# Performance work log

Measured on AMD Instinct MI355X. Metric: run time of the kernel, lower is better.

Reference implementation:

```python
import jax, jax.numpy as jnp
import numpy as np

N_NODES, N_EDGES, NNZ = 50000, 5000, 250000
IN_DIM, EDGE_DIM, N_HEADS, D_HEAD = 256, 256, 8, 64
OC = N_HEADS * D_HEAD  # out_channel = 512
EPS = 1e-5


def _segment_softmax(scores, seg, num_segments):
    # scores: [nnz, h]; softmax over entries sharing the same segment id
    m = jax.ops.segment_max(scores, seg, num_segments=num_segments)
    ex = jnp.exp(scores - m[seg])
    s = jax.ops.segment_sum(ex, seg, num_segments=num_segments)
    return ex / s[seg]


def _batchnorm(x, g, b):
    # BatchNorm1d in training mode: batch stats, biased variance
    mu = x.mean(axis=0)
    var = x.var(axis=0)
    return (x - mu) * jax.lax.rsqrt(var + EPS) * g + b


def setup_inputs() -> dict:
    key = jax.random.key(0)
    ks = jax.random.split(key, 26)
    W = lambda i, shape: (jax.random.normal(ks[i], shape, jnp.float32) * 0.05)
    inp = {
        "q": jax.random.normal(ks[0], (N_NODES, IN_DIM), jnp.float32),
        "k": jax.random.normal(ks[1], (N_NODES, IN_DIM), jnp.float32),
        "v": jax.random.normal(ks[2], (N_NODES, IN_DIM), jnp.float32),
        "edge_feat": jax.random.normal(ks[3], (N_EDGES, EDGE_DIM), jnp.float32),
        "Wq_n2h": W(4, (IN_DIM, OC)),
        "Wk_n2h": W(5, (IN_DIM, OC)),
        "Wv_n2h": W(6, (IN_DIM, OC)),
        "Wo_n2h": W(7, (OC, OC)),
        "We": W(8, (EDGE_DIM, IN_DIM)),
        "Wq_h2n": W(9, (IN_DIM, OC)),
        "Wk_h2n": W(10, (OC, OC)),
        "Wv_h2n": W(11, (OC, OC)),
        "Wo_h2n": W(12, (OC, OC)),
        "W1": W(13, (OC, 4 * OC)),
        "b1": jnp.zeros((4 * OC,), jnp.float32),
        "W2": W(14, (4 * OC, OC)),
        "b2": jnp.zeros((OC,), jnp.float32),
        "Wres": W(15, (IN_DIM, OC)),
        "g1": jnp.ones((OC,), jnp.float32),
        "beta1": jnp.zeros((OC,), jnp.float32),
        "g2": jnp.ones((OC,), jnp.float32),
        "beta2": jnp.zeros((OC,), jnp.float32),
        "node_ids": jax.random.randint(ks[16], (NNZ,), 0, N_NODES, jnp.int32),
        "hyperedge_ids": jax.random.randint(ks[17], (NNZ,), 0, N_EDGES, jnp.int32),
    }
    return inp


def reference(q, k, v, edge_feat, Wq_n2h, Wk_n2h, Wv_n2h, Wo_n2h, We,
              Wq_h2n, Wk_h2n, Wv_h2n, Wo_h2n, W1, b1, W2, b2, Wres,
              g1, beta1, g2, beta2, node_ids, hyperedge_ids):
    N, E = q.shape[0], edge_feat.shape[0]
    h, d = N_HEADS, D_HEAD
    scale = 1.0 / np.sqrt(d).astype(np.float32)

    # ---- node -> hyperedge attention (Q,V from node feats k; K from edge feats) ----
    edge_in = edge_feat @ We                                   # [E, in_dim]
    Q1 = (k @ Wq_n2h).reshape(N, h, d)
    K1 = (edge_in @ Wk_n2h).reshape(E, h, d)
    V1 = (k @ Wv_n2h).reshape(N, h, d)
    s1 = (Q1[node_ids] * K1[hyperedge_ids]).sum(-1) * scale    # [nnz, h]
    w1 = _segment_softmax(s1, hyperedge_ids, E)
    he = jax.ops.segment_sum(V1[node_ids] * w1[..., None], hyperedge_ids,
                             num_segments=E)                    # [E, h, d]
    he = he.reshape(E, h * d) @ Wo_n2h                          # [E, OC]

    # ---- hyperedge -> node attention (Q from node feats q; K,V from updated edges) ----
    Q2 = (q @ Wq_h2n).reshape(N, h, d)
    K2 = (he @ Wk_h2n).reshape(E, h, d)
    V2 = (he @ Wv_h2n).reshape(E, h, d)
    s2 = (Q2[node_ids] * K2[hyperedge_ids]).sum(-1) * scale
    w2 = _segment_softmax(s2, node_ids, N)
    nu = jax.ops.segment_sum(V2[hyperedge_ids] * w2[..., None], node_ids,
                             num_segments=N)                    # [N, h, d]
    nu = nu.reshape(N, h * d) @ Wo_h2n                          # [N, OC]

    # ---- residual + BN + FFN + residual + BN ----
    x = nu + q @ Wres
    x = _batchnorm(x, g1, beta1)
    ffn = jax.nn.gelu(x @ W1 + b1, approximate=False) @ W2 + b2
    return _batchnorm(x + ffn, g2, beta2)
```

## Files before the change

kernel.cpp:

```cpp
#include <hip/hip_runtime.h>
#include <math.h>
#include <stdint.h>

#define N_NODESC 50000
#define N_EDGESC 5000
#define NNZC     250000
#define IN_DIMC  256
#define OCC      512
#define NHC      8
#define EPSBN    1e-5f

typedef __attribute__((ext_vector_type(8))) short short8;
typedef __attribute__((ext_vector_type(4))) float f32x4;
typedef __attribute__((ext_vector_type(4))) unsigned short u16x4;
typedef unsigned short u16;

__device__ __forceinline__ u16 f2b(float f) {
    union { float f; unsigned u; } v; v.f = f;
    unsigned r = v.u + 0x7fffu + ((v.u >> 16) & 1u);
    return (u16)(r >> 16);
}

__device__ __forceinline__ void gload16(const u16* g, u16* l) {
    __builtin_amdgcn_global_load_lds(
        (const __attribute__((address_space(1))) unsigned int*)g,
        (__attribute__((address_space(3))) unsigned int*)l, 16, 0, 0);
}

__global__ __launch_bounds__(256)
void gemm_mfma(const u16* __restrict__ A, const u16* __restrict__ Bt,
               int M, int N, int K,
               const float* __restrict__ bias, int act,
               const float* resF, float* outF, u16* outB)
{
    __shared__ u16 As[128 * 64];
    __shared__ u16 Bs[128 * 64];
    const int tid  = threadIdx.x;
    const int wid  = tid >> 6, lane = tid & 63;
    const int wr   = wid >> 1, wc = wid & 1;
    const int m0   = blockIdx.y * 128, n0 = blockIdx.x * 128;

    f32x4 acc[4][4] = {};

    const int srow   = wid * 32 + (lane >> 3);
    const int schunk = (lane & 7) ^ ((lane >> 3) & 7);
    const int nk = K >> 6;

    for (int kt = 0; kt < nk; ++kt) {
        const int kb = kt * 64;
#pragma unroll
        for (int j = 0; j < 4; j++) {
            int gr = m0 + srow + j * 8;
            if (gr >= M) gr = M - 1;
            gload16(A + (size_t)gr * K + kb + schunk * 8, &As[(wid * 32 + j * 8) * 64]);
        }
#pragma unroll
        for (int j = 0; j < 4; j++) {
            int r = srow + j * 8;
            gload16(Bt + (size_t)(n0 + r) * K + kb + schunk * 8, &Bs[(wid * 32 + j * 8) * 64]);
        }
        __syncthreads();
#pragma unroll
        for (int ks = 0; ks < 2; ++ks) {
            short8 af[4], bfr[4];
#pragma unroll
            for (int mi = 0; mi < 4; mi++) {
                int r  = wr * 64 + mi * 16 + (lane & 15);
                int pc = ((lane >> 4) + ks * 4) ^ (r & 7);
                af[mi] = *(const short8*)&As[r * 64 + pc * 8];
            }
#pragma unroll
            for (int ni = 0; ni < 4; ni++) {
                int r  = wc * 64 + ni * 16 + (lane & 15);
                int pc = ((lane >> 4) + ks * 4) ^ (r & 7);
                bfr[ni] = *(const short8*)&Bs[r * 64 + pc * 8];
            }
#pragma unroll
            for (int mi = 0; mi < 4; mi++)
#pragma unroll
                for (int ni = 0; ni < 4; ni++)
                    acc[mi][ni] = __builtin_amdgcn_mfma_f32_16x16x32_bf16(
                        af[mi], bfr[ni], acc[mi][ni], 0, 0, 0);
        }
        __syncthreads();
    }

#pragma unroll
    for (int mi = 0; mi < 4; mi++) {
#pragma unroll
        for (int j = 0; j < 4; j++) {
            int row = m0 + wr * 64 + mi * 16 + (lane >> 4) * 4 + j;
            if (row >= M) continue;
#pragma unroll
            for (int ni = 0; ni < 4; ni++) {
                int col = n0 + wc * 64 + ni * 16 + (lane & 15);
                float v = acc[mi][ni][j];
                if (bias) v += bias[col];
                if (act)  v = 0.5f * v * (1.f + erff(v * 0.70710678118654752f));
                size_t o = (size_t)row * N + col;
                if (resF) v += resF[o];
                if (outF) outF[o] = v;
                if (outB) outB[o] = f2b(v);
            }
        }
    }
}

__global__ __launch_bounds__(256)
void wcast_kernel(const float* __restrict__ W, u16* __restrict__ Wt, int K, int N)
{
    __shared__ float t[32][33];
    int k0 = blockIdx.y * 32, n0 = blockIdx.x * 32;
    int tx = threadIdx.x & 31, ty = threadIdx.x >> 5;
    for (int i = ty; i < 32; i += 8)
        t[i][tx] = W[(size_t)(k0 + i) * N + n0 + tx];
    __syncthreads();
    for (int i = ty; i < 32; i += 8)
        Wt[(size_t)(n0 + i) * K + k0 + tx] = f2b(t[tx][i]);
}

__global__ __launch_bounds__(256)
void cast_kernel(const float* __restrict__ in, u16* __restrict__ out, int n)
{
    int i = (blockIdx.x * 256 + threadIdx.x) * 4;
    if (i >= n) return;
    const float4 v = *(const float4*)(in + i);
    u16x4 o; o.x = f2b(v.x); o.y = f2b(v.y); o.z = f2b(v.z); o.w = f2b(v.w);
    *(u16x4*)(out + i) = o;
}

__device__ __forceinline__ unsigned f32_order(float f) {
    unsigned u = __float_as_uint(f);
    return (u & 0x80000000u) ? ~u : (u | 0x80000000u);
}
__device__ __forceinline__ float f32_unorder(unsigned u) {
    unsigned b = (u & 0x80000000u) ? (u & 0x7FFFFFFFu) : ~u;
    return __uint_as_float(b);
}

__global__ __launch_bounds__(64)
void score_kernel(const float* __restrict__ Qm, const int* __restrict__ qids,
                  const float* __restrict__ Km, const int* __restrict__ kids,
                  const int* __restrict__ segids,
                  float* __restrict__ sout, unsigned* __restrict__ segM)
{
    int i = blockIdx.x;
    int lane = threadIdx.x;
    const float* qp = Qm + (size_t)qids[i] * OCC;
    const float* kp = Km + (size_t)kids[i] * OCC;
    float prod[NHC];
#pragma unroll
    for (int j = 0; j < NHC; j++)
        prod[j] = qp[j * 64 + lane] * kp[j * 64 + lane];
#pragma unroll
    for (int j = 0; j < NHC; j++) {
        float v = prod[j];
        for (int o = 32; o > 0; o >>= 1) v += __shfl_xor(v, o, 64);
        prod[j] = v;
    }
    if (lane < NHC) {
        float s = 0.f;
#pragma unroll
        for (int j = 0; j < NHC; j++) if (lane == j) s = prod[j];
        s *= 0.125f;
        sout[(size_t)i * NHC + lane] = s;
        atomicMax(segM + (size_t)segids[i] * NHC + lane, f32_order(s));
    }
}

__global__ __launch_bounds__(256)
void expsum_kernel(float* __restrict__ s, const int* __restrict__ segids,
                   const unsigned* __restrict__ segM, float* __restrict__ segS,
                   int n)
{
    int idx = blockIdx.x * blockDim.x + threadIdx.x;
    if (idx >= n) return;
    int i = idx >> 3, j = idx & 7;
    int seg = segids[i];
    float m = f32_unorder(segM[(size_t)seg * NHC + j]);
    float e = expf(s[idx] - m);
    s[idx] = e;
    atomicAdd(segS + (size_t)seg * NHC + j, e);
}

__global__ __launch_bounds__(64)
void scatter_kernel(const float* __restrict__ Vm, const int* __restrict__ vids,
                    const int* __restrict__ dids, const float* __restrict__ ex,
                    float* acc)
{
    int i = blockIdx.x;
    int lane = threadIdx.x;
    const float* vp = Vm + (size_t)vids[i] * OCC;
    float* ap = acc + (size_t)dids[i] * OCC;
    const float* exr = ex + (size_t)i * NHC;
#pragma unroll
    for (int j = 0; j < NHC; j++)
        atomicAdd(ap + j * 64 + lane, vp[j * 64 + lane] * exr[j]);
}

__global__ __launch_bounds__(256)
void norm_seg_b_kernel(const float* __restrict__ acc, const float* __restrict__ segS,
                       u16* __restrict__ outb, int n)
{
    int idx = blockIdx.x * blockDim.x + threadIdx.x;
    if (idx >= n) return;
    int r = idx >> 9;
    int c = idx & 511;
    float s = segS[(size_t)r * NHC + (c >> 6)];
    outb[idx] = f2b((s > 0.f) ? acc[idx] / s : 0.f);
}

__global__ __launch_bounds__(256)
void bn_stats_kernel(const float* __restrict__ x, float* sums, float* sumsq,
                     int rows)
{
    int t = threadIdx.x;
    float s0 = 0.f, s1 = 0.f, q0 = 0.f, q1 = 0.f;
    for (int r = blockIdx.x; r < rows; r += gridDim.x) {
        const float* xp = x + (size_t)r * OCC;
        float a = xp[t], b = xp[t + 256];
        s0 += a; q0 += a * a;
        s1 += b; q1 += b * b;
    }
    atomicAdd(&sums[t], s0);
    atomicAdd(&sums[t + 256], s1);
    atomicAdd(&sumsq[t], q0);
    atomicAdd(&sumsq[t + 256], q1);
}

__global__ __launch_bounds__(256)
void bn_apply_kernel(const float* __restrict__ x, const float* __restrict__ sums,
                     const float* __restrict__ sumsq, const float* __restrict__ g,
                     const float* __restrict__ b, float* y, int rows)
{
    int idx = blockIdx.x * blockDim.x + threadIdx.x;
    if (idx >= rows * OCC) return;
    int c = idx & 511;
    float inv_n = 1.f / (float)rows;
    float mu = sums[c] * inv_n;
    float var = sumsq[c] * inv_n - mu * mu;
    float rstd = rsqrtf(var + EPSBN);
    y[idx] = (x[idx] - mu) * rstd * g[c] + b[c];
}


static inline void launch_mfma(const u16* A, const u16* Bt, int M, int N, int K,
                               const float* bias, int act, const float* resF,
                               float* outF, u16* outB, hipStream_t s)
{
    dim3 g(N / 128, (M + 127) / 128);
    hipLaunchKernelGGL(gemm_mfma, g, dim3(256), 0, s, A, Bt, M, N, K,
                       bias, act, resF, outF, outB);
}
static inline void launch_wcast(const float* W, u16* Wt, int K, int N, hipStream_t s)
{
    hipLaunchKernelGGL(wcast_kernel, dim3(N / 32, K / 32), dim3(256), 0, s, W, Wt, K, N);
}
static inline void launch_cast(const float* in, u16* out, int n, hipStream_t s)
{
    hipLaunchKernelGGL(cast_kernel, dim3((n / 4 + 255) / 256), dim3(256), 0, s, in, out, n);
}

extern "C" void kernel_launch(void* const* d_in, const int* in_sizes, int n_in,
                              void* d_out, int out_size, void* d_ws, size_t ws_size,
                              hipStream_t stream)
{
    const float* q         = (const float*)d_in[0];
    const float* k         = (const float*)d_in[1];
    const float* edge_feat = (const float*)d_in[3];
    const float* Wq_n2h    = (const float*)d_in[4];
    const float* Wk_n2h    = (const float*)d_in[5];
    const float* Wv_n2h    = (const float*)d_in[6];
    const float* Wo_n2h    = (const float*)d_in[7];
    const float* We        = (const float*)d_in[8];
    const float* Wq_h2n    = (const float*)d_in[9];
    const float* Wk_h2n    = (const float*)d_in[10];
    const float* Wv_h2n    = (const float*)d_in[11];
    const float* Wo_h2n    = (const float*)d_in[12];
    const float* W1        = (const float*)d_in[13];
    const float* b1        = (const float*)d_in[14];
    const float* W2        = (const float*)d_in[15];
    const float* b2        = (const float*)d_in[16];
    const float* Wres      = (const float*)d_in[17];
    const float* g1        = (const float*)d_in[18];
    const float* beta1     = (const float*)d_in[19];
    const float* g2        = (const float*)d_in[20];
    const float* beta2     = (const float*)d_in[21];
    const int*   node_ids      = (const int*)d_in[22];
    const int*   hyperedge_ids = (const int*)d_in[23];
    float* out = (float*)d_out;
    (void)in_sizes; (void)n_in; (void)out_size;

    float* ws = (float*)d_ws;
    size_t off = 0;
    auto allocF = [&](size_t n) { off = (off + 3) & ~(size_t)3; float* p = ws + off; off += n; return p; };
    auto allocB = [&](size_t nelem) { return (u16*)allocF((nelem + 1) / 2); };

    float* bufB  = allocF((size_t)N_NODESC * OCC);
    float* bufE1 = allocF((size_t)N_EDGESC * OCC);
    float* bufE2 = allocF((size_t)N_EDGESC * OCC);
    u16*   heAB  = allocB((size_t)N_EDGESC * OCC);
    u16*   heB   = allocB((size_t)N_EDGESC * OCC);
    u16*   eiB   = allocB((size_t)N_EDGESC * IN_DIMC);
    float* sEx   = allocF((size_t)NNZC * NHC);
    unsigned* segM = (unsigned*)allocF((size_t)N_NODESC * NHC);
    float* segS  = allocF((size_t)N_NODESC * NHC);
    float* bnstat= allocF(4 * OCC);
    u16*   kB    = allocB((size_t)N_NODESC * IN_DIMC);
    u16*   qB    = allocB((size_t)N_NODESC * IN_DIMC);
    u16*   nuB   = kB;

    u16* WeT  = allocB(256 * 256);
    u16* WqnT = allocB(512 * 256);
    u16* WknT = allocB(512 * 256);
    u16* WvnT = allocB(512 * 256);
    u16* WonT = allocB(512 * 512);
    u16* WqhT = allocB(512 * 256);
    u16* WkhT = allocB(512 * 512);
    u16* WvhT = allocB(512 * 512);
    u16* WohT = allocB(512 * 512);
    u16* W1T  = allocB(2048 * 512);
    u16* W2T  = allocB(512 * 2048);
    u16* WrT  = allocB(512 * 256);

    size_t ws_floats = ws_size / sizeof(float);
    size_t remain = (ws_floats > off + 8) ? (ws_floats - off - 8) : 0;
    long ch = (long)(remain / 1280);
    if (ch > 12800) ch = 12800;
    if (ch < 1024)  ch = 1024;
    int CH = (int)ch;
    u16* xbC  = allocB((size_t)CH * OCC);
    u16* ffnB = allocB((size_t)CH * 4 * OCC);

    float* Qbuf = out;
    float* sums1 = bnstat, *sq1 = bnstat + OCC, *sums2 = bnstat + 2 * OCC, *sq2 = bnstat + 3 * OCC;

    launch_wcast(We,     WeT,  256, 256, stream);
    launch_wcast(Wq_n2h, WqnT, 256, 512, stream);
    launch_wcast(Wk_n2h, WknT, 256, 512, stream);
    launch_wcast(Wv_n2h, WvnT, 256, 512, stream);
    launch_wcast(Wo_n2h, WonT, 512, 512, stream);
    launch_wcast(Wq_h2n, WqhT, 256, 512, stream);
    launch_wcast(Wk_h2n, WkhT, 512, 512, stream);
    launch_wcast(Wv_h2n, WvhT, 512, 512, stream);
    launch_wcast(Wo_h2n, WohT, 512, 512, stream);
    launch_wcast(W1,     W1T,  512, 2048, stream);
    launch_wcast(W2,     W2T,  2048, 512, stream);
    launch_wcast(Wres,   WrT,  256, 512, stream);
    launch_cast(k, kB, N_NODESC * IN_DIMC, stream);
    launch_cast(q, qB, N_NODESC * IN_DIMC, stream);

    u16* efB = (CH * OCC >= N_EDGESC * IN_DIMC) ? xbC : heB;
    launch_cast(edge_feat, efB, N_EDGESC * IN_DIMC, stream);

    hipMemsetAsync(segM, 0, (size_t)N_NODESC * NHC * 4, stream);
    hipMemsetAsync(segS, 0, (size_t)N_NODESC * NHC * 4, stream);
    hipMemsetAsync(bufE2, 0, (size_t)N_EDGESC * OCC * 4, stream);
    hipMemsetAsync(bnstat, 0, 4 * OCC * 4, stream);

    launch_mfma(efB, WeT, N_EDGESC, IN_DIMC, IN_DIMC, nullptr, 0, nullptr, nullptr, eiB, stream);
    launch_mfma(kB, WqnT, N_NODESC, OCC, IN_DIMC, nullptr, 0, nullptr, Qbuf, nullptr, stream);
    launch_mfma(eiB, WknT, N_EDGESC, OCC, IN_DIMC, nullptr, 0, nullptr, bufE1, nullptr, stream);
    launch_mfma(kB, WvnT, N_NODESC, OCC, IN_DIMC, nullptr, 0, nullptr, bufB, nullptr, stream);

    hipLaunchKernelGGL(score_kernel, dim3(NNZC), dim3(64), 0, stream,
                       Qbuf, node_ids, bufE1, hyperedge_ids, hyperedge_ids, sEx, segM);
    hipLaunchKernelGGL(expsum_kernel, dim3((NNZC * NHC + 255) / 256), dim3(256), 0, stream,
                       sEx, hyperedge_ids, segM, segS, NNZC * NHC);
    hipLaunchKernelGGL(scatter_kernel, dim3(NNZC), dim3(64), 0, stream,
                       bufB, node_ids, hyperedge_ids, sEx, bufE2);
    hipLaunchKernelGGL(norm_seg_b_kernel, dim3((N_EDGESC * OCC + 255) / 256), dim3(256), 0, stream,
                       bufE2, segS, heAB, N_EDGESC * OCC);
    launch_mfma(heAB, WonT, N_EDGESC, OCC, OCC, nullptr, 0, nullptr, nullptr, heB, stream);

    launch_mfma(qB, WqhT, N_NODESC, OCC, IN_DIMC, nullptr, 0, nullptr, Qbuf, nullptr, stream);
    launch_mfma(heB, WkhT, N_EDGESC, OCC, OCC, nullptr, 0, nullptr, bufE1, nullptr, stream);
    launch_mfma(heB, WvhT, N_EDGESC, OCC, OCC, nullptr, 0, nullptr, bufE2, nullptr, stream);

    hipMemsetAsync(segM, 0, (size_t)N_NODESC * NHC * 4, stream);
    hipMemsetAsync(segS, 0, (size_t)N_NODESC * NHC * 4, stream);

    hipLaunchKernelGGL(score_kernel, dim3(NNZC), dim3(64), 0, stream,
                       Qbuf, node_ids, bufE1, hyperedge_ids, node_ids, sEx, segM);

    launch_mfma(qB, WrT, N_NODESC, OCC, IN_DIMC, nullptr, 0, nullptr, Qbuf, nullptr, stream);

    hipMemsetAsync(bufB, 0, (size_t)N_NODESC * OCC * 4, stream);

    hipLaunchKernelGGL(expsum_kernel, dim3((NNZC * NHC + 255) / 256), dim3(256), 0, stream,
                       sEx, node_ids, segM, segS, NNZC * NHC);
    hipLaunchKernelGGL(scatter_kernel, dim3(NNZC), dim3(64), 0, stream,
                       bufE2, hyperedge_ids, node_ids, sEx, bufB);
    hipLaunchKernelGGL(norm_seg_b_kernel, dim3((N_NODESC * OCC + 255) / 256), dim3(256), 0, stream,
                       bufB, segS, nuB, N_NODESC * OCC);

    launch_mfma(nuB, WohT, N_NODESC, OCC, OCC, nullptr, 0, Qbuf, Qbuf, nullptr, stream);

    hipLaunchKernelGGL(bn_stats_kernel, dim3(512), dim3(256), 0, stream, Qbuf, sums1, sq1, N_NODESC);
    hipLaunchKernelGGL(bn_apply_kernel, dim3((N_NODESC * OCC + 255) / 256), dim3(256), 0, stream,
                       Qbuf, sums1, sq1, g1, beta1, Qbuf, N_NODESC);

    for (int c0 = 0; c0 < N_NODESC; c0 += CH) {
        int mrows = (N_NODESC - c0 < CH) ? (N_NODESC - c0) : CH;
        const float* xc = Qbuf + (size_t)c0 * OCC;
        launch_cast(xc, xbC, mrows * OCC, stream);
        launch_mfma(xbC, W1T, mrows, 4 * OCC, OCC, b1, 1, nullptr, nullptr, ffnB, stream);
        launch_mfma(ffnB, W2T, mrows, OCC, 4 * OCC, b2, 0, xc, bufB + (size_t)c0 * OCC, nullptr, stream);
    }

    hipLaunchKernelGGL(bn_stats_kernel, dim3(512), dim3(256), 0, stream, bufB, sums2, sq2, N_NODESC);
    hipLaunchKernelGGL(bn_apply_kernel, dim3((N_NODESC * OCC + 255) / 256), dim3(256), 0, stream,
                       bufB, sums2, sq2, g2, beta2, out, N_NODESC);
}
```

Baseline: 2.904 ms.

## Replace atomic scatter softmax with CSR-sorted fused online-softmax segment attention

Builds CSR segment offsets and permutations with histogram, scan and fill kernels, then computes each segment's attention in one fused pass using an online softmax (one block per hyperedge, one wave per node). This removes the score, expsum, atomic scatter and normalize kernels, along with their float atomics and intermediate buffers. It adds a single-block serial scan over 50000 entries and per-segment load imbalance, and changes the order of the floating-point sums.

```diff
diff --git a/kernel.cpp b/kernel.cpp
--- a/kernel.cpp
+++ b/kernel.cpp
@@ -129,85 +129,164 @@
     *(u16x4*)(out + i) = o;
 }
 
-__device__ __forceinline__ unsigned f32_order(float f) {
-    unsigned u = __float_as_uint(f);
-    return (u & 0x80000000u) ? ~u : (u | 0x80000000u);
-}
-__device__ __forceinline__ float f32_unorder(unsigned u) {
-    unsigned b = (u & 0x80000000u) ? (u & 0x7FFFFFFFu) : ~u;
-    return __uint_as_float(b);
-}
-
-__global__ __launch_bounds__(64)
-void score_kernel(const float* __restrict__ Qm, const int* __restrict__ qids,
-                  const float* __restrict__ Km, const int* __restrict__ kids,
-                  const int* __restrict__ segids,
-                  float* __restrict__ sout, unsigned* __restrict__ segM)
-{
-    int i = blockIdx.x;
-    int lane = threadIdx.x;
-    const float* qp = Qm + (size_t)qids[i] * OCC;
-    const float* kp = Km + (size_t)kids[i] * OCC;
-    float prod[NHC];
-#pragma unroll
-    for (int j = 0; j < NHC; j++)
-        prod[j] = qp[j * 64 + lane] * kp[j * 64 + lane];
-#pragma unroll
-    for (int j = 0; j < NHC; j++) {
-        float v = prod[j];
-        for (int o = 32; o > 0; o >>= 1) v += __shfl_xor(v, o, 64);
-        prod[j] = v;
-    }
-    if (lane < NHC) {
-        float s = 0.f;
-#pragma unroll
-        for (int j = 0; j < NHC; j++) if (lane == j) s = prod[j];
-        s *= 0.125f;
-        sout[(size_t)i * NHC + lane] = s;
-        atomicMax(segM + (size_t)segids[i] * NHC + lane, f32_order(s));
-    }
-}
-
-__global__ __launch_bounds__(256)
-void expsum_kernel(float* __restrict__ s, const int* __restrict__ segids,
-                   const unsigned* __restrict__ segM, float* __restrict__ segS,
-                   int n)
-{
-    int idx = blockIdx.x * blockDim.x + threadIdx.x;
-    if (idx >= n) return;
-    int i = idx >> 3, j = idx & 7;
-    int seg = segids[i];
-    float m = f32_unorder(segM[(size_t)seg * NHC + j]);
-    float e = expf(s[idx] - m);
-    s[idx] = e;
-    atomicAdd(segS + (size_t)seg * NHC + j, e);
-}
-
-__global__ __launch_bounds__(64)
-void scatter_kernel(const float* __restrict__ Vm, const int* __restrict__ vids,
-                    const int* __restrict__ dids, const float* __restrict__ ex,
-                    float* acc)
-{
-    int i = blockIdx.x;
-    int lane = threadIdx.x;
-    const float* vp = Vm + (size_t)vids[i] * OCC;
-    float* ap = acc + (size_t)dids[i] * OCC;
-    const float* exr = ex + (size_t)i * NHC;
-#pragma unroll
-    for (int j = 0; j < NHC; j++)
-        atomicAdd(ap + j * 64 + lane, vp[j * 64 + lane] * exr[j]);
-}
-
-__global__ __launch_bounds__(256)
-void norm_seg_b_kernel(const float* __restrict__ acc, const float* __restrict__ segS,
-                       u16* __restrict__ outb, int n)
-{
-    int idx = blockIdx.x * blockDim.x + threadIdx.x;
-    if (idx >= n) return;
-    int r = idx >> 9;
-    int c = idx & 511;
-    float s = segS[(size_t)r * NHC + (c >> 6)];
-    outb[idx] = f2b((s > 0.f) ? acc[idx] / s : 0.f);
+__global__ __launch_bounds__(256)
+void hist_kernel(const int* __restrict__ ids, int n, int* counts)
+{
+    int i = blockIdx.x * 256 + threadIdx.x;
+    if (i < n) atomicAdd(&counts[ids[i]], 1);
+}
+
+__global__ __launch_bounds__(1024)
+void scan_kernel(const int* __restrict__ counts, int* __restrict__ offs, int n)
+{
+    __shared__ int tmp[1024];
+    __shared__ int carry;
+    int tid = threadIdx.x;
+    if (tid == 0) carry = 0;
+    __syncthreads();
+    for (int base = 0; base < n; base += 1024) {
+        int v = (base + tid < n) ? counts[base + tid] : 0;
+        tmp[tid] = v;
+        __syncthreads();
+        for (int o = 1; o < 1024; o <<= 1) {
+            int t = (tid >= o) ? tmp[tid - o] : 0;
+            __syncthreads();
+            tmp[tid] += t;
+            __syncthreads();
+        }
+        if (base + tid < n) offs[base + tid] = carry + tmp[tid] - v;
+        __syncthreads();
+        if (tid == 0) carry += tmp[1023];
+        __syncthreads();
+    }
+    if (tid == 0) offs[n] = carry;
+}
+
+__global__ __launch_bounds__(256)
+void fill_kernel(const int* __restrict__ ids, int n, const int* __restrict__ offs,
+                 int* cursor, int* __restrict__ perm)
+{
+    int i = blockIdx.x * 256 + threadIdx.x;
+    if (i >= n) return;
+    int s = ids[i];
+    int p = atomicAdd(&cursor[s], 1);
+    perm[offs[s] + p] = i;
+}
+
+__global__ __launch_bounds__(256)
+void seg_attn_block(const float* __restrict__ F, const float* __restrict__ G,
+                    const float* __restrict__ V, const int* __restrict__ gid,
+                    const int* __restrict__ offs, const int* __restrict__ perm,
+                    u16* __restrict__ outB)
+{
+    __shared__ float sm[4][NHC], sl[4][NHC], sacc[4][NHC][64];
+    const int seg = blockIdx.x;
+    const int lane = threadIdx.x & 63, wid = threadIdx.x >> 6;
+    const int beg = offs[seg], end = offs[seg + 1];
+
+    float f[NHC], m[NHC], l[NHC], acc[NHC];
+#pragma unroll
+    for (int h = 0; h < NHC; h++) {
+        f[h] = F[(size_t)seg * OCC + h * 64 + lane];
+        m[h] = -INFINITY; l[h] = 0.f; acc[h] = 0.f;
+    }
+
+    for (int i = beg + wid; i < end; i += 4) {
+        int id = gid[perm[i]];
+        const float* gp = G + (size_t)id * OCC;
+        const float* vp = V + (size_t)id * OCC;
+        float gv[NHC], vv[NHC], s[NHC];
+#pragma unroll
+        for (int h = 0; h < NHC; h++) gv[h] = gp[h * 64 + lane];
+#pragma unroll
+        for (int h = 0; h < NHC; h++) vv[h] = vp[h * 64 + lane];
+#pragma unroll
+        for (int h = 0; h < NHC; h++) {
+            float p = f[h] * gv[h];
+#pragma unroll
+            for (int o = 32; o > 0; o >>= 1) p += __shfl_xor(p, o, 64);
+            s[h] = p * 0.125f;
+        }
+#pragma unroll
+        for (int h = 0; h < NHC; h++) {
+            float mn = fmaxf(m[h], s[h]);
+            float sc = __expf(m[h] - mn);
+            float w  = __expf(s[h] - mn);
+            l[h]   = l[h] * sc + w;
+            acc[h] = acc[h] * sc + w * vv[h];
+            m[h]   = mn;
+        }
+    }
+
+#pragma unroll
+    for (int h = 0; h < NHC; h++) {
+        if (lane == h) { sm[wid][h] = m[h]; sl[wid][h] = l[h]; }
+        sacc[wid][h][lane] = acc[h];
+    }
+    __syncthreads();
+
+    for (int e = threadIdx.x; e < OCC; e += 256) {
+        int h = e >> 6, ln = e & 63;
+        float M = fmaxf(fmaxf(sm[0][h], sm[1][h]), fmaxf(sm[2][h], sm[3][h]));
+        float L = 0.f, A = 0.f;
+#pragma unroll
+        for (int w = 0; w < 4; w++) {
+            float sc = __expf(sm[w][h] - M);
+            L += sl[w][h] * sc;
+            A += sacc[w][h][ln] * sc;
+        }
+        outB[(size_t)seg * OCC + e] = f2b((L > 0.f) ? A / L : 0.f);
+    }
+}
+
+__global__ __launch_bounds__(256)
+void seg_attn_wave(const float* __restrict__ F, const float* __restrict__ G,
+                   const float* __restrict__ V, const int* __restrict__ gid,
+                   const int* __restrict__ offs, const int* __restrict__ perm,
+                   u16* __restrict__ outB, int nseg)
+{
+    const int seg = blockIdx.x * 4 + (threadIdx.x >> 6);
+    if (seg >= nseg) return;
+    const int lane = threadIdx.x & 63;
+    const int beg = offs[seg], end = offs[seg + 1];
+
+    float f[NHC], m[NHC], l[NHC], acc[NHC];
+#pragma unroll
+    for (int h = 0; h < NHC; h++) {
+        f[h] = F[(size_t)seg * OCC + h * 64 + lane];
+        m[h] = -INFINITY; l[h] = 0.f; acc[h] = 0.f;
+    }
+
+    for (int i = beg; i < end; ++i) {
+        int id = gid[perm[i]];
+        const float* gp = G + (size_t)id * OCC;
+        const float* vp = V + (size_t)id * OCC;
+        float gv[NHC], vv[NHC], s[NHC];
+#pragma unroll
+        for (int h = 0; h < NHC; h++) gv[h] = gp[h * 64 + lane];
+#pragma unroll
+        for (int h = 0; h < NHC; h++) vv[h] = vp[h * 64 + lane];
+#pragma unroll
+        for (int h = 0; h < NHC; h++) {
+            float p = f[h] * gv[h];
+#pragma unroll
+            for (int o = 32; o > 0; o >>= 1) p += __shfl_xor(p, o, 64);
+            s[h] = p * 0.125f;
+        }
+#pragma unroll
+        for (int h = 0; h < NHC; h++) {
+            float mn = fmaxf(m[h], s[h]);
+            float sc = __expf(m[h] - mn);
+            float w  = __expf(s[h] - mn);
+            l[h]   = l[h] * sc + w;
+            acc[h] = acc[h] * sc + w * vv[h];
+            m[h]   = mn;
+        }
+    }
+
+#pragma unroll
+    for (int h = 0; h < NHC; h++)
+        outB[(size_t)seg * OCC + h * 64 + lane] = f2b((l[h] > 0.f) ? acc[h] / l[h] : 0.f);
 }
 
 __global__ __launch_bounds__(256)
@@ -295,6 +374,7 @@
     size_t off = 0;
     auto allocF = [&](size_t n) { off = (off + 3) & ~(size_t)3; float* p = ws + off; off += n; return p; };
     auto allocB = [&](size_t nelem) { return (u16*)allocF((nelem + 1) / 2); };
+    auto allocI = [&](size_t n) { return (int*)allocF(n); };
 
     float* bufB  = allocF((size_t)N_NODESC * OCC);
     float* bufE1 = allocF((size_t)N_EDGESC * OCC);
@@ -302,13 +382,19 @@
     u16*   heAB  = allocB((size_t)N_EDGESC * OCC);
     u16*   heB   = allocB((size_t)N_EDGESC * OCC);
     u16*   eiB   = allocB((size_t)N_EDGESC * IN_DIMC);
-    float* sEx   = allocF((size_t)NNZC * NHC);
-    unsigned* segM = (unsigned*)allocF((size_t)N_NODESC * NHC);
-    float* segS  = allocF((size_t)N_NODESC * NHC);
     float* bnstat= allocF(4 * OCC);
     u16*   kB    = allocB((size_t)N_NODESC * IN_DIMC);
     u16*   qB    = allocB((size_t)N_NODESC * IN_DIMC);
     u16*   nuB   = kB;
+
+    int* cnt1  = allocI(N_EDGESC);
+    int* cur1  = allocI(N_EDGESC);
+    int* offs1 = allocI(N_EDGESC + 4);
+    int* perm1 = allocI(NNZC);
+    int* cnt2  = allocI(N_NODESC);
+    int* cur2  = allocI(N_NODESC);
+    int* offs2 = allocI(N_NODESC + 4);
+    int* perm2 = allocI(NNZC);
 
     u16* WeT  = allocB(256 * 256);
     u16* WqnT = allocB(512 * 256);
@@ -349,52 +435,45 @@
     launch_wcast(Wres,   WrT,  256, 512, stream);
     launch_cast(k, kB, N_NODESC * IN_DIMC, stream);
     launch_cast(q, qB, N_NODESC * IN_DIMC, stream);
-
     u16* efB = (CH * OCC >= N_EDGESC * IN_DIMC) ? xbC : heB;
     launch_cast(edge_feat, efB, N_EDGESC * IN_DIMC, stream);
 
-    hipMemsetAsync(segM, 0, (size_t)N_NODESC * NHC * 4, stream);
-    hipMemsetAsync(segS, 0, (size_t)N_NODESC * NHC * 4, stream);
-    hipMemsetAsync(bufE2, 0, (size_t)N_EDGESC * OCC * 4, stream);
+    hipMemsetAsync(cnt1, 0, N_EDGESC * 4, stream);
+    hipMemsetAsync(cur1, 0, N_EDGESC * 4, stream);
+    hipMemsetAsync(cnt2, 0, N_NODESC * 4, stream);
+    hipMemsetAsync(cur2, 0, N_NODESC * 4, stream);
     hipMemsetAsync(bnstat, 0, 4 * OCC * 4, stream);
+
+    hipLaunchKernelGGL(hist_kernel, dim3((NNZC + 255) / 256), dim3(256), 0, stream,
+                       hyperedge_ids, NNZC, cnt1);
+    hipLaunchKernelGGL(scan_kernel, dim3(1), dim3(1024), 0, stream, cnt1, offs1, N_EDGESC);
+    hipLaunchKernelGGL(fill_kernel, dim3((NNZC + 255) / 256), dim3(256), 0, stream,
+                       hyperedge_ids, NNZC, offs1, cur1, perm1);
+    hipLaunchKernelGGL(hist_kernel, dim3((NNZC + 255) / 256), dim3(256), 0, stream,
+                       node_ids, NNZC, cnt2);
+    hipLaunchKernelGGL(scan_kernel, dim3(1), dim3(1024), 0, stream, cnt2, offs2, N_NODESC);
+    hipLaunchKernelGGL(fill_kernel, dim3((NNZC + 255) / 256), dim3(256), 0, stream,
+                       node_ids, NNZC, offs2, cur2, perm2);
 
     launch_mfma(efB, WeT, N_EDGESC, IN_DIMC, IN_DIMC, nullptr, 0, nullptr, nullptr, eiB, stream);
     launch_mfma(kB, WqnT, N_NODESC, OCC, IN_DIMC, nullptr, 0, nullptr, Qbuf, nullptr, stream);
     launch_mfma(eiB, WknT, N_EDGESC, OCC, IN_DIMC, nullptr, 0, nullptr, bufE1, nullptr, stream);
     launch_mfma(kB, WvnT, N_NODESC, OCC, IN_DIMC, nullptr, 0, nullptr, bufB, nullptr, stream);
 
-    hipLaunchKernelGGL(score_kernel, dim3(NNZC), dim3(64), 0, stream,
-                       Qbuf, node_ids, bufE1, hyperedge_ids, hyperedge_ids, sEx, segM);
-    hipLaunchKernelGGL(expsum_kernel, dim3((NNZC * NHC + 255) / 256), dim3(256), 0, stream,
-                       sEx, hyperedge_ids, segM, segS, NNZC * NHC);
-    hipLaunchKernelGGL(scatter_kernel, dim3(NNZC), dim3(64), 0, stream,
-                       bufB, node_ids, hyperedge_ids, sEx, bufE2);
-    hipLaunchKernelGGL(norm_seg_b_kernel, dim3((N_EDGESC * OCC + 255) / 256), dim3(256), 0, stream,
-                       bufE2, segS, heAB, N_EDGESC * OCC);
+    hipLaunchKernelGGL(seg_attn_block, dim3(N_EDGESC), dim3(256), 0, stream,
+                       bufE1 , Qbuf , bufB , node_ids, offs1, perm1, heAB);
     launch_mfma(heAB, WonT, N_EDGESC, OCC, OCC, nullptr, 0, nullptr, nullptr, heB, stream);
 
     launch_mfma(qB, WqhT, N_NODESC, OCC, IN_DIMC, nullptr, 0, nullptr, Qbuf, nullptr, stream);
     launch_mfma(heB, WkhT, N_EDGESC, OCC, OCC, nullptr, 0, nullptr, bufE1, nullptr, stream);
     launch_mfma(heB, WvhT, N_EDGESC, OCC, OCC, nullptr, 0, nullptr, bufE2, nullptr, stream);
-
-    hipMemsetAsync(segM, 0, (size_t)N_NODESC * NHC * 4, stream);
-    hipMemsetAsync(segS, 0, (size_t)N_NODESC * NHC * 4, stream);
-
-    hipLaunchKernelGGL(score_kernel, dim3(NNZC), dim3(64), 0, stream,
-                       Qbuf, node_ids, bufE1, hyperedge_ids, node_ids, sEx, segM);
-
-    launch_mfma(qB, WrT, N_NODESC, OCC, IN_DIMC, nullptr, 0, nullptr, Qbuf, nullptr, stream);
-
-    hipMemsetAsync(bufB, 0, (size_t)N_NODESC * OCC * 4, stream);
-
-    hipLaunchKernelGGL(expsum_kernel, dim3((NNZC * NHC + 255) / 256), dim3(256), 0, stream,
-                       sEx, node_ids, segM, segS, NNZC * NHC);
-    hipLaunchKernelGGL(scatter_kernel, dim3(NNZC), dim3(64), 0, stream,
-                       bufE2, hyperedge_ids, node_ids, sEx, bufB);
-    hipLaunchKernelGGL(norm_seg_b_kernel, dim3((N_NODESC * OCC + 255) / 256), dim3(256), 0, stream,
-                       bufB, segS, nuB, N_NODESC * OCC);
-
-    launch_mfma(nuB, WohT, N_NODESC, OCC, OCC, nullptr, 0, Qbuf, Qbuf, nullptr, stream);
+    launch_mfma(qB, WrT, N_NODESC, OCC, IN_DIMC, nullptr, 0, nullptr, bufB, nullptr, stream);
+
+    hipLaunchKernelGGL(seg_attn_wave, dim3((N_NODESC + 3) / 4), dim3(256), 0, stream,
+                       Qbuf , bufE1 , bufE2 , hyperedge_ids, offs2, perm2,
+                       nuB, N_NODESC);
+
+    launch_mfma(nuB, WohT, N_NODESC, OCC, OCC, nullptr, 0, bufB, Qbuf, nullptr, stream);
 
     hipLaunchKernelGGL(bn_stats_kernel, dim3(512), dim3(256), 0, stream, Qbuf, sums1, sq1, N_NODESC);
     hipLaunchKernelGGL(bn_apply_kernel, dim3((N_NODESC * OCC + 255) / 256), dim3(256), 0, stream,
```

New measurement: 2.411 ms. 17.0% less time.
